# Kernel optimization log

Hardware: AMD Instinct MI355X
Metric: run time of the kernel (lower is better)

## Reference

```python
import jax, jax.numpy as jnp
import numpy as np

V, E, H, Z, T = 8185, 353, 191, 13, 25
START = 19


def _lstm(x, h, c, k, rk, b):
    # Keras LSTMCell: gates ordered i, f, g(candidate), o
    gates = x @ k + h @ rk + b                      # (B, 4H)
    i, f, g, o = jnp.split(gates, 4, axis=-1)
    c_new = jax.nn.sigmoid(f) * c + jax.nn.sigmoid(i) * jnp.tanh(g)
    h_new = jax.nn.sigmoid(o) * jnp.tanh(c_new)
    return h_new, c_new


def setup_inputs() -> dict:
    key = jax.random.key(0)
    ks = jax.random.split(key, 18)
    B = 256
    s = 0.05
    inp = {
        "inputs": jax.random.randint(ks[0], (B, T), 0, V),
        "epsilon": jax.random.normal(ks[1], (Z,), jnp.float32),
        "emb": jax.random.normal(ks[2], (V, E), jnp.float32) * s,
        "inf_k": jax.random.normal(ks[3], (E, 4 * H), jnp.float32) * s,
        "inf_rk": jax.random.normal(ks[4], (H, 4 * H), jnp.float32) * s,
        "inf_b": jnp.zeros((4 * H,), jnp.float32),
        "mu_w": jax.random.normal(ks[5], (H, Z), jnp.float32) * s,
        "mu_b": jnp.zeros((Z,), jnp.float32),
        "sig_w": jax.random.normal(ks[6], (H, Z), jnp.float32) * s,
        "sig_b": jnp.zeros((Z,), jnp.float32),
        "init_w": jax.random.normal(ks[7], (Z, H), jnp.float32) * s,
        "init_b": jnp.zeros((H,), jnp.float32),
        "gen_k": jax.random.normal(ks[8], (E, 4 * H), jnp.float32) * s,
        "gen_rk": jax.random.normal(ks[9], (H, 4 * H), jnp.float32) * s,
        "gen_b": jnp.zeros((4 * H,), jnp.float32),
        "out_w": jax.random.normal(ks[10], (H, V), jnp.float32) * s,
        "out_b": jnp.zeros((V,), jnp.float32),
    }
    return inp


def reference(inputs, epsilon, emb, inf_k, inf_rk, inf_b, mu_w, mu_b,
              sig_w, sig_b, init_w, init_b, gen_k, gen_rk, gen_b,
              out_w, out_b):
    B = inputs.shape[0]
    # ----- encoder (inference LSTM over the full sequence) -----
    inf_emb = emb[inputs]                             # (B, T, E)

    def enc_step(carry, x_t):
        h, c = carry
        h, c = _lstm(x_t, h, c, inf_k, inf_rk, inf_b)
        return (h, c), None

    h0 = jnp.zeros((B, H), emb.dtype)
    (h_enc, _), _ = jax.lax.scan(enc_step, (h0, h0),
                                 jnp.swapaxes(inf_emb, 0, 1))  # scan over T

    mu = h_enc @ mu_w + mu_b                          # (B, Z)
    sigma = h_enc @ sig_w + sig_b                     # (B, Z)
    z = mu + epsilon * sigma                          # shared epsilon (Z,)

    init_state = z @ init_w + init_b                  # (B, H)
    emb0 = jnp.broadcast_to(emb[START], (B, E))       # start token embedding

    def dec_step(carry, _):
        h, c, x = carry
        h, c = _lstm(x, h, c, gen_k, gen_rk, gen_b)
        logits = h @ out_w + out_b                    # (B, V)
        new_ind = jnp.argmax(logits, axis=-1)         # (B,)
        x_next = emb[new_ind]                         # (B, E)
        return (h, c, x_next), logits

    _, logits_seq = jax.lax.scan(dec_step, (init_state, init_state, emb0),
                                 None, length=T)      # (T, B, V)
    return jnp.swapaxes(logits_seq, 0, 1)             # (B, T, V)
```

## Files before the change

kernel.cpp:

```cpp
#include <hip/hip_runtime.h>
#include <math.h>

#define V_  8185
#define E_  353
#define H_  191
#define FH_ 764
#define Z_  13
#define T_  25
#define START_ 19
#define VP_ 8192
#define NTL 64
#define RKS 192

__device__ __forceinline__ float sigf(float x) { return 1.0f / (1.0f + expf(-x)); }

__global__ __launch_bounds__(256) void pad_w_kernel(const float* __restrict__ src,
                                                    float* __restrict__ dst) {
  int i = blockIdx.x * 256 + threadIdx.x;
  if (i >= H_ * VP_) return;
  int k = i >> 13;
  int j = i & (VP_ - 1);
  dst[i] = (j < V_) ? src[(size_t)k * V_ + j] : 0.0f;
}

__global__ __launch_bounds__(256) void transpose_rk(const float* __restrict__ rkA,
                                                    const float* __restrict__ rkB,
                                                    float* __restrict__ dst) {
  int i = blockIdx.x * 256 + threadIdx.x;
  if (i >= 2 * FH_ * RKS) return;
  int w = i / (FH_ * RKS), rem = i - w * (FH_ * RKS);
  int col4 = rem / RKS, k = rem - col4 * RKS;
  const float* src = w ? rkB : rkA;
  dst[i] = (k < H_) ? src[(size_t)k * FH_ + col4] : 0.0f;
}

__global__ __launch_bounds__(256) void gemm_ew(const float* __restrict__ emb,
                                               const float* __restrict__ W,
                                               float* __restrict__ C, int M,
                                               const int* __restrict__ inputs,
                                               int mode, int B) {
  __shared__ __align__(16) float AT[E_ * 16];
  const int tid = threadIdx.x;
  const int n0 = blockIdx.x * 256;
  const int m0 = blockIdx.y * 16;
  for (int i = tid; i < 16 * E_; i += 256) {
    int r = i / E_, k = i - r * E_;
    int m = m0 + r;
    float v = 0.0f;
    if (m < M) {
      int row;
      if (mode == 0) row = m;
      else { int t = m / B, b = m - t * B; row = inputs[b * T_ + t]; }
      v = emb[(size_t)row * E_ + k];
    }
    AT[k * 16 + r] = v;
  }
  __syncthreads();
  const int lane = tid & 63;
  const int w4 = (tid >> 6) * 4;
  const int j = n0 + lane * 4;
  if (j >= FH_) return;
  float4 c0 = {0,0,0,0}, c1 = {0,0,0,0}, c2 = {0,0,0,0}, c3 = {0,0,0,0};
  const float* wc = W + j;
  const float* at = AT + w4;
  for (int k = 0; k < E_; ++k) {
    float4 wv = *(const float4*)(wc + (size_t)k * FH_);
    float4 a  = *(const float4*)(at + k * 16);
    c0.x = fmaf(a.x, wv.x, c0.x); c0.y = fmaf(a.x, wv.y, c0.y);
    c0.z = fmaf(a.x, wv.z, c0.z); c0.w = fmaf(a.x, wv.w, c0.w);
    c1.x = fmaf(a.y, wv.x, c1.x); c1.y = fmaf(a.y, wv.y, c1.y);
    c1.z = fmaf(a.y, wv.z, c1.z); c1.w = fmaf(a.y, wv.w, c1.w);
    c2.x = fmaf(a.z, wv.x, c2.x); c2.y = fmaf(a.z, wv.y, c2.y);
    c2.z = fmaf(a.z, wv.z, c2.z); c2.w = fmaf(a.z, wv.w, c2.w);
    c3.x = fmaf(a.w, wv.x, c3.x); c3.y = fmaf(a.w, wv.y, c3.y);
    c3.z = fmaf(a.w, wv.z, c3.z); c3.w = fmaf(a.w, wv.w, c3.w);
  }
  const int mb = m0 + w4;
  if (mb + 0 < M) *(float4*)(C + (size_t)(mb + 0) * FH_ + j) = c0;
  if (mb + 1 < M) *(float4*)(C + (size_t)(mb + 1) * FH_ + j) = c1;
  if (mb + 2 < M) *(float4*)(C + (size_t)(mb + 2) * FH_ + j) = c2;
  if (mb + 3 < M) *(float4*)(C + (size_t)(mb + 3) * FH_ + j) = c3;
}

__global__ __launch_bounds__(256) void lstm_step(const float* __restrict__ xk,
                                                 const float* __restrict__ rkT,
                                                 const float* __restrict__ bias,
                                                 const float* __restrict__ h_in,
                                                 const float* __restrict__ c_in,
                                                 float* __restrict__ h_out,
                                                 float* __restrict__ c_out,
                                                 const float* __restrict__ pmax,
                                                 const int* __restrict__ pidx,
                                                 int mode, int first) {
  __shared__ float rks[32][193];
  __shared__ __align__(16) float hs[16][RKS];
  __shared__ float xs[16 * 32];
  __shared__ float bs[32];
  __shared__ int   tk[16];
  __shared__ float pv[16 * NTL];
  __shared__ int   pi[16 * NTL];
  __shared__ float gb[32 * 16];

  const int tid = threadIdx.x;
  const int c0 = blockIdx.x * 8;
  const int m0 = blockIdx.y * 16;

  if (mode) {
    if (first) {
      if (tid < 16) tk[tid] = START_;
    } else {
      for (int i = tid; i < 16 * NTL; i += 256) {
        int row = i >> 6, s = i & (NTL - 1);
        pv[i] = pmax[(size_t)(m0 + row) * NTL + s];
        pi[i] = pidx[(size_t)(m0 + row) * NTL + s];
      }
      __syncthreads();
      if (tid < 16) {
        float bv = pv[tid * NTL]; int bi = pi[tid * NTL];
        for (int s = 1; s < NTL; ++s) {
          float v = pv[tid * NTL + s]; int ii = pi[tid * NTL + s];
          if (v > bv || (v == bv && ii < bi)) { bv = v; bi = ii; }
        }
        tk[tid] = bi;
      }
    }
    __syncthreads();
  }

  for (int i = tid; i < 32 * 48; i += 256) {
    int qq = i / 48, kq = (i - qq * 48) * 4;
    int jj2 = c0 + (qq & 7), g = qq >> 3;
    float4 v = {0, 0, 0, 0};
    if (jj2 < H_) v = *(const float4*)(rkT + (size_t)(jj2 + H_ * g) * RKS + kq);
    rks[qq][kq]     = v.x; rks[qq][kq + 1] = v.y;
    rks[qq][kq + 2] = v.z; rks[qq][kq + 3] = v.w;
  }
  for (int i = tid; i < 16 * H_; i += 256) {
    int r = i / H_, k = i - r * H_;
    hs[r][k] = h_in[(size_t)m0 * H_ + i];
  }
  for (int i = tid; i < 16 * 32; i += 256) {
    int row = i >> 5, q = i & 31;
    int jj = c0 + (q & 7);
    int jg = jj + H_ * (q >> 3);
    float xv = 0.0f;
    if (jj < H_) {
      const float* xrow = mode ? (xk + (size_t)tk[row] * FH_)
                               : (xk + (size_t)(m0 + row) * FH_);
      xv = xrow[jg];
    }
    xs[i] = xv;
  }
  if (tid < 32) {
    int jj = c0 + (tid & 7);
    bs[tid] = (jj < H_) ? bias[jj + H_ * (tid >> 3)] : 0.0f;
  }
  __syncthreads();

  const int q = tid & 31, rg = tid >> 5;
  const int jj = c0 + (q & 7);
  float a0 = 0.0f, a1 = 0.0f;
  if (jj < H_) {
    const float* rr  = rks[q];
    const float* h0p = hs[rg];
    const float* h1p = hs[rg + 8];
    int k = 0;
    for (; k < 188; k += 4) {
      float4 h0v = *(const float4*)(h0p + k);
      float4 h1v = *(const float4*)(h1p + k);
      float w0 = rr[k], w1 = rr[k + 1], w2 = rr[k + 2], w3 = rr[k + 3];
      a0 = fmaf(h0v.x, w0, a0); a1 = fmaf(h1v.x, w0, a1);
      a0 = fmaf(h0v.y, w1, a0); a1 = fmaf(h1v.y, w1, a1);
      a0 = fmaf(h0v.z, w2, a0); a1 = fmaf(h1v.z, w2, a1);
      a0 = fmaf(h0v.w, w3, a0); a1 = fmaf(h1v.w, w3, a1);
    }
    for (; k < H_; ++k) {
      float wv = rr[k];
      a0 = fmaf(h0p[k], wv, a0);
      a1 = fmaf(h1p[k], wv, a1);
    }
  }
  gb[q * 16 + rg] = a0;
  gb[q * 16 + rg + 8] = a1;
  __syncthreads();

  if (tid < 128) {
    int cc = tid & 7, row = tid >> 3;
    int jc = c0 + cc;
    if (jc < H_) {
      float gi = gb[(cc      ) * 16 + row] + xs[row * 32 + cc      ] + bs[cc];
      float gf = gb[( 8 + cc ) * 16 + row] + xs[row * 32 +  8 + cc ] + bs[ 8 + cc];
      float gg = gb[(16 + cc ) * 16 + row] + xs[row * 32 + 16 + cc ] + bs[16 + cc];
      float go = gb[(24 + cc ) * 16 + row] + xs[row * 32 + 24 + cc ] + bs[24 + cc];
      float co = c_in[(size_t)(m0 + row) * H_ + jc];
      float cn = sigf(gf) * co + sigf(gi) * tanhf(gg);
      float hn = sigf(go) * tanhf(cn);
      c_out[(size_t)(m0 + row) * H_ + jc] = cn;
      h_out[(size_t)(m0 + row) * H_ + jc] = hn;
    }
  }
}

__global__ __launch_bounds__(256) void logits_argmax(const float* __restrict__ h,
                                                     const float* __restrict__ wp,
                                                     const float* __restrict__ ob,
                                                     float* __restrict__ out, int t,
                                                     float* __restrict__ pmax,
                                                     int* __restrict__ pidx) {
  __shared__ __align__(16) float AT[H_ * 36];
  const int tid = threadIdx.x;
  const int n0 = blockIdx.x * 128;
  const int m0 = blockIdx.y * 32;
  for (int i = tid; i < 32 * H_; i += 256) {
    int r = i / H_, k = i - r * H_;
    AT[k * 36 + r] = h[(size_t)m0 * H_ + i];
  }
  __syncthreads();

  const int cq = tid & 31;
  const int ro = tid >> 5;
  const int j = n0 + cq * 4;
  float4 acc[4] = {{0,0,0,0},{0,0,0,0},{0,0,0,0},{0,0,0,0}};
  const float* wc = wp + j;
  const float* at = AT + ro * 4;
  for (int k = 0; k < H_; ++k) {
    float4 wv = *(const float4*)(wc + (size_t)k * VP_);
    float4 a  = *(const float4*)(at + k * 36);
    acc[0].x = fmaf(a.x, wv.x, acc[0].x); acc[0].y = fmaf(a.x, wv.y, acc[0].y);
    acc[0].z = fmaf(a.x, wv.z, acc[0].z); acc[0].w = fmaf(a.x, wv.w, acc[0].w);
    acc[1].x = fmaf(a.y, wv.x, acc[1].x); acc[1].y = fmaf(a.y, wv.y, acc[1].y);
    acc[1].z = fmaf(a.y, wv.z, acc[1].z); acc[1].w = fmaf(a.y, wv.w, acc[1].w);
    acc[2].x = fmaf(a.z, wv.x, acc[2].x); acc[2].y = fmaf(a.z, wv.y, acc[2].y);
    acc[2].z = fmaf(a.z, wv.z, acc[2].z); acc[2].w = fmaf(a.z, wv.w, acc[2].w);
    acc[3].x = fmaf(a.w, wv.x, acc[3].x); acc[3].y = fmaf(a.w, wv.y, acc[3].y);
    acc[3].z = fmaf(a.w, wv.z, acc[3].z); acc[3].w = fmaf(a.w, wv.w, acc[3].w);
  }

  float bias4[4];
#pragma unroll
  for (int u = 0; u < 4; ++u) bias4[u] = (j + u < V_) ? ob[j + u] : 0.0f;
  const bool tile_full = (n0 + 128 <= V_);
#pragma unroll
  for (int rr = 0; rr < 4; ++rr) {
    const int b = m0 + ro * 4 + rr;
    float v[4] = {acc[rr].x + bias4[0], acc[rr].y + bias4[1],
                  acc[rr].z + bias4[2], acc[rr].w + bias4[3]};
    float* orow = out + ((size_t)b * T_ + t) * V_ + j;
    if (tile_full) {
      orow[0] = v[0]; orow[1] = v[1]; orow[2] = v[2]; orow[3] = v[3];
    } else {
#pragma unroll
      for (int u = 0; u < 4; ++u)
        if (j + u < V_) orow[u] = v[u];
    }
    float bv = -INFINITY; int bi = 0;
#pragma unroll
    for (int u = 0; u < 4; ++u)
      if (j + u < V_ && v[u] > bv) { bv = v[u]; bi = j + u; }
#pragma unroll
    for (int off = 1; off < 32; off <<= 1) {
      float ov = __shfl_xor(bv, off, 64);
      int   oi = __shfl_xor(bi, off, 64);
      if (ov > bv || (ov == bv && oi < bi)) { bv = ov; bi = oi; }
    }
    if ((tid & 31) == 0) {
      pmax[(size_t)b * NTL + blockIdx.x] = bv;
      pidx[(size_t)b * NTL + blockIdx.x] = bi;
    }
  }
}

__global__ __launch_bounds__(64) void latent_k(const float* __restrict__ h,
                                               const float* __restrict__ eps,
                                               const float* __restrict__ mu_w,
                                               const float* __restrict__ mu_b,
                                               const float* __restrict__ sig_w,
                                               const float* __restrict__ sig_b,
                                               const float* __restrict__ iw,
                                               const float* __restrict__ ib,
                                               float* __restrict__ h0,
                                               float* __restrict__ c0) {
  __shared__ float zs[4 * Z_];
  const int tid = threadIdx.x;
  const int m0 = blockIdx.x * 4;
  if (tid < 4 * Z_) {
    int row = tid / Z_, qz = tid - row * Z_;
    const float* hr = h + (size_t)(m0 + row) * H_;
    float mu = mu_b[qz], sg = sig_b[qz];
    for (int k = 0; k < H_; ++k) {
      float hv = hr[k];
      mu = fmaf(hv, mu_w[k * Z_ + qz], mu);
      sg = fmaf(hv, sig_w[k * Z_ + qz], sg);
    }
    zs[tid] = mu + eps[qz] * sg;
  }
  __syncthreads();
  for (int i = tid; i < 4 * H_; i += 64) {
    int row = i / H_, col = i - row * H_;
    float acc = ib[col];
#pragma unroll
    for (int qz = 0; qz < Z_; ++qz)
      acc = fmaf(zs[row * Z_ + qz], iw[qz * H_ + col], acc);
    h0[(size_t)(m0 + row) * H_ + col] = acc;
    c0[(size_t)(m0 + row) * H_ + col] = acc;
  }
}

extern "C" void kernel_launch(void* const* d_in, const int* in_sizes, int n_in,
                              void* d_out, int out_size, void* d_ws, size_t ws_size,
                              hipStream_t stream) {
  const int*   inputs = (const int*)  d_in[0];
  const float* eps    = (const float*)d_in[1];
  const float* emb    = (const float*)d_in[2];
  const float* inf_k  = (const float*)d_in[3];
  const float* inf_rk = (const float*)d_in[4];
  const float* inf_b  = (const float*)d_in[5];
  const float* mu_w   = (const float*)d_in[6];
  const float* mu_b   = (const float*)d_in[7];
  const float* sig_w  = (const float*)d_in[8];
  const float* sig_b  = (const float*)d_in[9];
  const float* init_w = (const float*)d_in[10];
  const float* init_b = (const float*)d_in[11];
  const float* gen_k  = (const float*)d_in[12];
  const float* gen_rk = (const float*)d_in[13];
  const float* gen_b  = (const float*)d_in[14];
  const float* out_w  = (const float*)d_in[15];
  const float* out_b  = (const float*)d_in[16];
  float* out = (float*)d_out;

  const int B = in_sizes[0] / T_;
  const int BH = B * H_;

  float* ws = (float*)d_ws;
  size_t off = 0;
  float* EK = ws + off; off += (size_t)V_ * FH_;
  float* XK = ws + off; off += (size_t)T_ * B * FH_;
  float* WP = ws + off; off += (size_t)H_ * VP_;
  float* rkT = ws + off; off += (size_t)2 * FH_ * RKS;
  float* hbase = ws + off; off += (size_t)8 * BH;
  float* he[2] = {hbase + 0 * BH, hbase + 2 * BH};
  float* ce[2] = {hbase + 1 * BH, hbase + 3 * BH};
  float* hd[2] = {hbase + 4 * BH, hbase + 6 * BH};
  float* cd[2] = {hbase + 5 * BH, hbase + 7 * BH};
  float* pmax = ws + off; off += (size_t)B * NTL;
  int*   pidx = (int*)(ws + off); off += (size_t)B * NTL;
  float* rkT_inf = rkT;
  float* rkT_gen = rkT + (size_t)FH_ * RKS;

  hipMemsetAsync(hbase, 0, (size_t)2 * BH * sizeof(float), stream);

  pad_w_kernel<<<(H_ * VP_ + 255) / 256, 256, 0, stream>>>(out_w, WP);
  transpose_rk<<<(2 * FH_ * RKS + 255) / 256, 256, 0, stream>>>(inf_rk, gen_rk, rkT);
  gemm_ew<<<dim3(3, (V_ + 15) / 16), 256, 0, stream>>>(emb, gen_k, EK, V_, nullptr, 0, B);
  gemm_ew<<<dim3(3, (T_ * B) / 16), 256, 0, stream>>>(emb, inf_k, XK, T_ * B, inputs, 1, B);

  for (int t = 0; t < T_; ++t) {
    lstm_step<<<dim3(24, B / 16), 256, 0, stream>>>(
        XK + (size_t)t * B * FH_, rkT_inf, inf_b,
        he[t & 1], ce[t & 1], he[(t + 1) & 1], ce[(t + 1) & 1],
        nullptr, nullptr, 0, 0);
  }

  latent_k<<<B / 4, 64, 0, stream>>>(he[T_ & 1], eps, mu_w, mu_b, sig_w, sig_b,
                                     init_w, init_b, hd[0], cd[0]);

  for (int t = 0; t < T_; ++t) {
    lstm_step<<<dim3(24, B / 16), 256, 0, stream>>>(
        EK, rkT_gen, gen_b,
        hd[t & 1], cd[t & 1], hd[(t + 1) & 1], cd[(t + 1) & 1],
        pmax, pidx, 1, (t == 0) ? 1 : 0);
    logits_argmax<<<dim3(NTL, B / 32), 256, 0, stream>>>(
        hd[(t + 1) & 1], WP, out_b, out, t, pmax, pidx);
  }
}
```

Measured before the change: 1.724 ms.

## Halve per-block batch rows in LSTM and logits kernels, parallelize argmax merge

Halves the batch rows handled per block in the LSTM step (16 to 8) and in the logits/argmax kernel (32 to 16), doubling the grid size so more CUs are busy in these latency-bound sequential steps. The cross-tile argmax merge now runs on 32 threads in two stages instead of 16 serial threads. The logits loop adds software prefetch of the next weight row, and the two weight-prep kernels are merged into one launch. In exchange, each weight tile is re-read from global or L2 by twice as many blocks, with less register reuse per block.

```diff
diff --git a/kernel.cpp b/kernel.cpp
--- a/kernel.cpp
+++ b/kernel.cpp
@@ -14,24 +14,25 @@
 
 __device__ __forceinline__ float sigf(float x) { return 1.0f / (1.0f + expf(-x)); }
 
-__global__ __launch_bounds__(256) void pad_w_kernel(const float* __restrict__ src,
-                                                    float* __restrict__ dst) {
+__global__ __launch_bounds__(256) void prep_w(const float* __restrict__ ow,
+                                              const float* __restrict__ rkA,
+                                              const float* __restrict__ rkB,
+                                              float* __restrict__ WP,
+                                              float* __restrict__ rkT) {
   int i = blockIdx.x * 256 + threadIdx.x;
-  if (i >= H_ * VP_) return;
-  int k = i >> 13;
-  int j = i & (VP_ - 1);
-  dst[i] = (j < V_) ? src[(size_t)k * V_ + j] : 0.0f;
-}
-
-__global__ __launch_bounds__(256) void transpose_rk(const float* __restrict__ rkA,
-                                                    const float* __restrict__ rkB,
-                                                    float* __restrict__ dst) {
-  int i = blockIdx.x * 256 + threadIdx.x;
-  if (i >= 2 * FH_ * RKS) return;
-  int w = i / (FH_ * RKS), rem = i - w * (FH_ * RKS);
-  int col4 = rem / RKS, k = rem - col4 * RKS;
-  const float* src = w ? rkB : rkA;
-  dst[i] = (k < H_) ? src[(size_t)k * FH_ + col4] : 0.0f;
+  if (i < H_ * VP_) {
+    int k = i >> 13;
+    int j = i & (VP_ - 1);
+    WP[i] = (j < V_) ? ow[(size_t)k * V_ + j] : 0.0f;
+  } else {
+    int i2 = i - H_ * VP_;
+    if (i2 < 2 * FH_ * RKS) {
+      int w = i2 / (FH_ * RKS), rem = i2 - w * (FH_ * RKS);
+      int col4 = rem / RKS, k = rem - col4 * RKS;
+      const float* src = w ? rkB : rkA;
+      rkT[i2] = (k < H_) ? src[(size_t)k * FH_ + col4] : 0.0f;
+    }
+  }
 }
 
 __global__ __launch_bounds__(256) void gemm_ew(const float* __restrict__ emb,
@@ -93,32 +94,45 @@
                                                  const int* __restrict__ pidx,
                                                  int mode, int first) {
   __shared__ float rks[32][193];
-  __shared__ __align__(16) float hs[16][RKS];
-  __shared__ float xs[16 * 32];
+  __shared__ __align__(16) float hs[8][RKS];
+  __shared__ float xs[8 * 32];
   __shared__ float bs[32];
-  __shared__ int   tk[16];
-  __shared__ float pv[16 * NTL];
-  __shared__ int   pi[16 * NTL];
-  __shared__ float gb[32 * 16];
+  __shared__ int   tk[8];
+  __shared__ float pv[8 * NTL];
+  __shared__ int   pi[8 * NTL];
+  __shared__ float cbv[8][4];
+  __shared__ int   cbi[8][4];
+  __shared__ float gb[32 * 8];
 
   const int tid = threadIdx.x;
   const int c0 = blockIdx.x * 8;
-  const int m0 = blockIdx.y * 16;
+  const int m0 = blockIdx.y * 8;
 
   if (mode) {
     if (first) {
-      if (tid < 16) tk[tid] = START_;
+      if (tid < 8) tk[tid] = START_;
     } else {
-      for (int i = tid; i < 16 * NTL; i += 256) {
+      for (int i = tid; i < 8 * NTL; i += 256) {
         int row = i >> 6, s = i & (NTL - 1);
         pv[i] = pmax[(size_t)(m0 + row) * NTL + s];
         pi[i] = pidx[(size_t)(m0 + row) * NTL + s];
       }
       __syncthreads();
-      if (tid < 16) {
-        float bv = pv[tid * NTL]; int bi = pi[tid * NTL];
-        for (int s = 1; s < NTL; ++s) {
-          float v = pv[tid * NTL + s]; int ii = pi[tid * NTL + s];
+      if (tid < 32) {
+        int row = tid >> 2, cch = tid & 3;
+        int base = row * NTL + cch * 16;
+        float bv = pv[base]; int bi = pi[base];
+        for (int s = 1; s < 16; ++s) {
+          float v = pv[base + s]; int ii = pi[base + s];
+          if (v > bv || (v == bv && ii < bi)) { bv = v; bi = ii; }
+        }
+        cbv[row][cch] = bv; cbi[row][cch] = bi;
+      }
+      __syncthreads();
+      if (tid < 8) {
+        float bv = cbv[tid][0]; int bi = cbi[tid][0];
+        for (int cch = 1; cch < 4; ++cch) {
+          float v = cbv[tid][cch]; int ii = cbi[tid][cch];
           if (v > bv || (v == bv && ii < bi)) { bv = v; bi = ii; }
         }
         tk[tid] = bi;
@@ -135,11 +149,12 @@
     rks[qq][kq]     = v.x; rks[qq][kq + 1] = v.y;
     rks[qq][kq + 2] = v.z; rks[qq][kq + 3] = v.w;
   }
-  for (int i = tid; i < 16 * H_; i += 256) {
+  for (int i = tid; i < 8 * H_; i += 256) {
     int r = i / H_, k = i - r * H_;
     hs[r][k] = h_in[(size_t)m0 * H_ + i];
   }
-  for (int i = tid; i < 16 * 32; i += 256) {
+  {
+    int i = tid;
     int row = i >> 5, q = i & 31;
     int jj = c0 + (q & 7);
     int jg = jj + H_ * (q >> 3);
@@ -159,39 +174,31 @@
 
   const int q = tid & 31, rg = tid >> 5;
   const int jj = c0 + (q & 7);
-  float a0 = 0.0f, a1 = 0.0f;
+  float a0 = 0.0f;
   if (jj < H_) {
-    const float* rr  = rks[q];
-    const float* h0p = hs[rg];
-    const float* h1p = hs[rg + 8];
+    const float* rr = rks[q];
+    const float* hp = hs[rg];
     int k = 0;
     for (; k < 188; k += 4) {
-      float4 h0v = *(const float4*)(h0p + k);
-      float4 h1v = *(const float4*)(h1p + k);
-      float w0 = rr[k], w1 = rr[k + 1], w2 = rr[k + 2], w3 = rr[k + 3];
-      a0 = fmaf(h0v.x, w0, a0); a1 = fmaf(h1v.x, w0, a1);
-      a0 = fmaf(h0v.y, w1, a0); a1 = fmaf(h1v.y, w1, a1);
-      a0 = fmaf(h0v.z, w2, a0); a1 = fmaf(h1v.z, w2, a1);
-      a0 = fmaf(h0v.w, w3, a0); a1 = fmaf(h1v.w, w3, a1);
-    }
-    for (; k < H_; ++k) {
-      float wv = rr[k];
-      a0 = fmaf(h0p[k], wv, a0);
-      a1 = fmaf(h1p[k], wv, a1);
-    }
-  }
-  gb[q * 16 + rg] = a0;
-  gb[q * 16 + rg + 8] = a1;
-  __syncthreads();
-
-  if (tid < 128) {
+      float4 hv = *(const float4*)(hp + k);
+      a0 = fmaf(hv.x, rr[k    ], a0);
+      a0 = fmaf(hv.y, rr[k + 1], a0);
+      a0 = fmaf(hv.z, rr[k + 2], a0);
+      a0 = fmaf(hv.w, rr[k + 3], a0);
+    }
+    for (; k < H_; ++k) a0 = fmaf(hp[k], rr[k], a0);
+  }
+  gb[q * 8 + rg] = a0;
+  __syncthreads();
+
+  if (tid < 64) {
     int cc = tid & 7, row = tid >> 3;
     int jc = c0 + cc;
     if (jc < H_) {
-      float gi = gb[(cc      ) * 16 + row] + xs[row * 32 + cc      ] + bs[cc];
-      float gf = gb[( 8 + cc ) * 16 + row] + xs[row * 32 +  8 + cc ] + bs[ 8 + cc];
-      float gg = gb[(16 + cc ) * 16 + row] + xs[row * 32 + 16 + cc ] + bs[16 + cc];
-      float go = gb[(24 + cc ) * 16 + row] + xs[row * 32 + 24 + cc ] + bs[24 + cc];
+      float gi = gb[(cc     ) * 8 + row] + xs[row * 32 + cc     ] + bs[cc];
+      float gf = gb[( 8 + cc) * 8 + row] + xs[row * 32 +  8 + cc] + bs[ 8 + cc];
+      float gg = gb[(16 + cc) * 8 + row] + xs[row * 32 + 16 + cc] + bs[16 + cc];
+      float go = gb[(24 + cc) * 8 + row] + xs[row * 32 + 24 + cc] + bs[24 + cc];
       float co = c_in[(size_t)(m0 + row) * H_ + jc];
       float cn = sigf(gf) * co + sigf(gi) * tanhf(gg);
       float hn = sigf(go) * tanhf(cn);
@@ -207,44 +214,51 @@
                                                      float* __restrict__ out, int t,
                                                      float* __restrict__ pmax,
                                                      int* __restrict__ pidx) {
-  __shared__ __align__(16) float AT[H_ * 36];
+  __shared__ __align__(16) float AT[H_ * 20];
   const int tid = threadIdx.x;
   const int n0 = blockIdx.x * 128;
-  const int m0 = blockIdx.y * 32;
-  for (int i = tid; i < 32 * H_; i += 256) {
+  const int m0 = blockIdx.y * 16;
+  for (int i = tid; i < 16 * H_; i += 256) {
     int r = i / H_, k = i - r * H_;
-    AT[k * 36 + r] = h[(size_t)m0 * H_ + i];
+    AT[k * 20 + r] = h[(size_t)m0 * H_ + i];
   }
   __syncthreads();
 
   const int cq = tid & 31;
   const int ro = tid >> 5;
   const int j = n0 + cq * 4;
-  float4 acc[4] = {{0,0,0,0},{0,0,0,0},{0,0,0,0},{0,0,0,0}};
   const float* wc = wp + j;
-  const float* at = AT + ro * 4;
-  for (int k = 0; k < H_; ++k) {
-    float4 wv = *(const float4*)(wc + (size_t)k * VP_);
-    float4 a  = *(const float4*)(at + k * 36);
-    acc[0].x = fmaf(a.x, wv.x, acc[0].x); acc[0].y = fmaf(a.x, wv.y, acc[0].y);
-    acc[0].z = fmaf(a.x, wv.z, acc[0].z); acc[0].w = fmaf(a.x, wv.w, acc[0].w);
-    acc[1].x = fmaf(a.y, wv.x, acc[1].x); acc[1].y = fmaf(a.y, wv.y, acc[1].y);
-    acc[1].z = fmaf(a.y, wv.z, acc[1].z); acc[1].w = fmaf(a.y, wv.w, acc[1].w);
-    acc[2].x = fmaf(a.z, wv.x, acc[2].x); acc[2].y = fmaf(a.z, wv.y, acc[2].y);
-    acc[2].z = fmaf(a.z, wv.z, acc[2].z); acc[2].w = fmaf(a.z, wv.w, acc[2].w);
-    acc[3].x = fmaf(a.w, wv.x, acc[3].x); acc[3].y = fmaf(a.w, wv.y, acc[3].y);
-    acc[3].z = fmaf(a.w, wv.z, acc[3].z); acc[3].w = fmaf(a.w, wv.w, acc[3].w);
-  }
+  const float* at = AT + ro * 2;
+  float4 acc0 = {0,0,0,0}, acc1 = {0,0,0,0};
+
+#define LFMA(AK, WV) { \
+    float2 a_ = *(const float2*)(at + (AK) * 20); \
+    acc0.x = fmaf(a_.x, WV.x, acc0.x); acc0.y = fmaf(a_.x, WV.y, acc0.y); \
+    acc0.z = fmaf(a_.x, WV.z, acc0.z); acc0.w = fmaf(a_.x, WV.w, acc0.w); \
+    acc1.x = fmaf(a_.y, WV.x, acc1.x); acc1.y = fmaf(a_.y, WV.y, acc1.y); \
+    acc1.z = fmaf(a_.y, WV.z, acc1.z); acc1.w = fmaf(a_.y, WV.w, acc1.w); }
+
+  float4 w0 = *(const float4*)(wc);
+  int k = 0;
+  for (; k < 190; k += 2) {
+    float4 w1 = *(const float4*)(wc + (size_t)(k + 1) * VP_);
+    LFMA(k, w0)
+    w0 = *(const float4*)(wc + (size_t)(k + 2) * VP_);
+    LFMA(k + 1, w1)
+  }
+  LFMA(190, w0)
+#undef LFMA
 
   float bias4[4];
 #pragma unroll
   for (int u = 0; u < 4; ++u) bias4[u] = (j + u < V_) ? ob[j + u] : 0.0f;
   const bool tile_full = (n0 + 128 <= V_);
 #pragma unroll
-  for (int rr = 0; rr < 4; ++rr) {
-    const int b = m0 + ro * 4 + rr;
-    float v[4] = {acc[rr].x + bias4[0], acc[rr].y + bias4[1],
-                  acc[rr].z + bias4[2], acc[rr].w + bias4[3]};
+  for (int rr = 0; rr < 2; ++rr) {
+    const int b = m0 + ro * 2 + rr;
+    float4 acc = rr ? acc1 : acc0;
+    float v[4] = {acc.x + bias4[0], acc.y + bias4[1],
+                  acc.z + bias4[2], acc.w + bias4[3]};
     float* orow = out + ((size_t)b * T_ + t) * V_ + j;
     if (tile_full) {
       orow[0] = v[0]; orow[1] = v[1]; orow[2] = v[2]; orow[3] = v[3];
@@ -349,13 +363,13 @@
 
   hipMemsetAsync(hbase, 0, (size_t)2 * BH * sizeof(float), stream);
 
-  pad_w_kernel<<<(H_ * VP_ + 255) / 256, 256, 0, stream>>>(out_w, WP);
-  transpose_rk<<<(2 * FH_ * RKS + 255) / 256, 256, 0, stream>>>(inf_rk, gen_rk, rkT);
+  prep_w<<<(H_ * VP_ + 2 * FH_ * RKS + 255) / 256, 256, 0, stream>>>(
+      out_w, inf_rk, gen_rk, WP, rkT);
   gemm_ew<<<dim3(3, (V_ + 15) / 16), 256, 0, stream>>>(emb, gen_k, EK, V_, nullptr, 0, B);
   gemm_ew<<<dim3(3, (T_ * B) / 16), 256, 0, stream>>>(emb, inf_k, XK, T_ * B, inputs, 1, B);
 
   for (int t = 0; t < T_; ++t) {
-    lstm_step<<<dim3(24, B / 16), 256, 0, stream>>>(
+    lstm_step<<<dim3(24, B / 8), 256, 0, stream>>>(
         XK + (size_t)t * B * FH_, rkT_inf, inf_b,
         he[t & 1], ce[t & 1], he[(t + 1) & 1], ce[(t + 1) & 1],
         nullptr, nullptr, 0, 0);
@@ -365,11 +379,11 @@
                                      init_w, init_b, hd[0], cd[0]);
 
   for (int t = 0; t < T_; ++t) {
-    lstm_step<<<dim3(24, B / 16), 256, 0, stream>>>(
+    lstm_step<<<dim3(24, B / 8), 256, 0, stream>>>(
         EK, rkT_gen, gen_b,
         hd[t & 1], cd[t & 1], hd[(t + 1) & 1], cd[(t + 1) & 1],
         pmax, pidx, 1, (t == 0) ? 1 : 0);
-    logits_argmax<<<dim3(NTL, B / 32), 256, 0, stream>>>(
+    logits_argmax<<<dim3(NTL, B / 16), 256, 0, stream>>>(
         hd[(t + 1) & 1], WP, out_b, out, t, pmax, pidx);
   }
 }
```

New measurement: 1.726 ms. About the same (+0.1%).
